# Kernel tuning notes

Measured on AMD Instinct MI355X. Metric: run time of the kernel, lower is better.

The kernel has to match this reference:

```python
import jax, jax.numpy as jnp
import numpy as np

H, D = 16, 1024
HD = D // H  # 64

def setup_inputs() -> dict:
    key = jax.random.key(0)
    ks = jax.random.split(key, 11)
    B, S = 2, 2048
    s_in = 1.0 / np.sqrt(D)
    return {
        "V": jax.random.normal(ks[0], (B, S, D), jnp.float32),
        "K": jax.random.normal(ks[1], (B, S, D), jnp.float32),
        "Q": jax.random.normal(ks[2], (B, S, D), jnp.float32),
        # stacked per-head Linear weights, torch layout [out,in] -> [H, HD, D]
        "Wv": jax.random.normal(ks[3], (H, HD, D), jnp.float32) * s_in,
        "bv": jnp.zeros((H, HD), jnp.float32),
        "Wk": jax.random.normal(ks[4], (H, HD, D), jnp.float32) * s_in,
        "bk": jnp.zeros((H, HD), jnp.float32),
        "Wq": jax.random.normal(ks[5], (H, HD, D), jnp.float32) * s_in,
        "bq": jnp.zeros((H, HD), jnp.float32),
        "Wo": jax.random.normal(ks[6], (D, D), jnp.float32) * s_in,
        "bo": jnp.zeros((D,), jnp.float32),
    }

def reference(V, K, Q, Wv, bv, Wk, bk, Wq, bq, Wo, bo):
    scale = HD ** (-0.5)
    # per-head projections fused into one batched GEMM: [B,S,D] x [H,HD,D] -> [B,H,S,HD]
    q = jnp.einsum('bsd,hed->bhse', Q, Wq) + bq[None, :, None, :]
    k = jnp.einsum('bsd,hed->bhse', K, Wk) + bk[None, :, None, :]
    v = jnp.einsum('bsd,hed->bhse', V, Wv) + bv[None, :, None, :]
    # scaled dot-product attention
    scores = jnp.einsum('bhqe,bhke->bhqk', q, k) * scale  # [B,H,S,S]
    p = jax.nn.softmax(scores, axis=-1)
    att = jnp.einsum('bhqk,bhke->bhqe', p, v)  # [B,H,S,HD]
    # concat heads (head 0 first, matching the torch cat order) then output proj
    B, _, S, _ = att.shape
    cat = jnp.transpose(att, (0, 2, 1, 3)).reshape(B, S, H * HD)
    return cat @ Wo.T + bo
```

## Files before the change

### kernel.cpp

```cpp
#include <hip/hip_runtime.h>
#include <cstdint>
#include <cstddef>

typedef __bf16 bf16_t;
typedef bf16_t bf16x8 __attribute__((ext_vector_type(8)));
typedef float f32x4 __attribute__((ext_vector_type(4)));

__device__ __forceinline__ void gl_lds16(const void* g, void* l) {
  __builtin_amdgcn_global_load_lds(
      (const __attribute__((address_space(1))) void*)g,
      (__attribute__((address_space(3))) void*)l, 16, 0, 0);
}

__device__ __forceinline__ f32x4 mfma16(bf16x8 a, bf16x8 b, f32x4 c) {
  return __builtin_amdgcn_mfma_f32_16x16x32_bf16(a, b, c, 0, 0, 0);
}

struct CvtWArgs { const float* src[4]; };

__global__ __launch_bounds__(256) void convert_w(CvtWArgs a, bf16_t* __restrict__ dst) {
  unsigned g = blockIdx.x * 256u + threadIdx.x;
  unsigned seg = g >> 17, off = g & 0x1FFFFu;
  const float4* s = (const float4*)a.src[seg] + (size_t)off * 2;
  float4 x0 = s[0], x1 = s[1];
  bf16x8 o;
  o[0] = (bf16_t)x0.x; o[1] = (bf16_t)x0.y; o[2] = (bf16_t)x0.z; o[3] = (bf16_t)x0.w;
  o[4] = (bf16_t)x1.x; o[5] = (bf16_t)x1.y; o[6] = (bf16_t)x1.z; o[7] = (bf16_t)x1.w;
  *(bf16x8*)(dst + (size_t)g * 8) = o;
}

struct ProjArgs {
  const float* A[3]; const bf16_t* W[3]; const float* bias[3];
  bf16_t* out[3]; float scale[3];
};

__global__ __launch_bounds__(256, 3) void gemm_proj(ProjArgs p) {
  __shared__ __attribute__((aligned(16))) unsigned char smem[49152];
  float*  a_s = (float*)smem;
  bf16_t* b_s = (bf16_t*)(smem + 32768);
  const int K = 1024;
  const int z = blockIdx.z;
  const float*  A = p.A[z] + (size_t)blockIdx.x * 128 * K;
  const bf16_t* W = p.W[z] + (size_t)blockIdx.y * 128 * K;

  const int t = threadIdx.x;
  const int w = t >> 6, l = t & 63;
  const int lq = l >> 4, lr = l & 15;
  const int mq = w & 1, nq = w >> 1;

  f32x4 acc[4][4];
  f32x4 zero = {0.f, 0.f, 0.f, 0.f};
  #pragma unroll
  for (int i = 0; i < 4; i++)
    #pragma unroll
    for (int j = 0; j < 4; j++) acc[i][j] = zero;

  for (int k0 = 0; k0 < K; k0 += 64) {
    __syncthreads();
    #pragma unroll
    for (int i = 0; i < 8; i++) {
      int ci = t + i * 256;
      int r = ci >> 4, pc = ci & 15;
      int lc = pc ^ (r & 7);
      gl_lds16(A + (size_t)r * K + k0 + lc * 4, a_s + i * 1024 + w * 256);
    }
    #pragma unroll
    for (int i = 0; i < 4; i++) {
      int g = t + i * 256;
      int r = g >> 3, pc = g & 7;
      int lc = pc ^ (r & 7);
      gl_lds16(W + (size_t)r * K + k0 + lc * 8, b_s + i * 2048 + w * 512);
    }
    __syncthreads();
    #pragma unroll
    for (int kk = 0; kk < 2; kk++) {
      bf16x8 af[4], bfr[4];
      #pragma unroll
      for (int i = 0; i < 4; i++) {
        int R = mq * 64 + i * 16 + lr;
        int rx = R & 7;
        int c0 = kk * 8 + lq * 2;
        f32x4 lo = *(const f32x4*)(a_s + R * 64 + ((c0 ^ rx) << 2));
        f32x4 hi = *(const f32x4*)(a_s + R * 64 + (((c0 + 1) ^ rx) << 2));
        bf16x8 v;
        v[0] = (bf16_t)lo[0]; v[1] = (bf16_t)lo[1]; v[2] = (bf16_t)lo[2]; v[3] = (bf16_t)lo[3];
        v[4] = (bf16_t)hi[0]; v[5] = (bf16_t)hi[1]; v[6] = (bf16_t)hi[2]; v[7] = (bf16_t)hi[3];
        af[i] = v;
      }
      #pragma unroll
      for (int j = 0; j < 4; j++) {
        int R = nq * 64 + j * 16 + lr;
        int ch = (kk * 4 + lq) ^ (R & 7);
        bfr[j] = *(const bf16x8*)(b_s + R * 64 + ch * 8);
      }
      #pragma unroll
      for (int i = 0; i < 4; i++)
        #pragma unroll
        for (int j = 0; j < 4; j++)
          acc[i][j] = mfma16(af[i], bfr[j], acc[i][j]);
    }
  }

  const float* bias = p.bias[z];
  const float scale = p.scale[z];
  __syncthreads();
  bf16_t* ts = (bf16_t*)smem;
  #pragma unroll
  for (int i = 0; i < 4; i++) {
    #pragma unroll
    for (int j = 0; j < 4; j++) {
      int nl = nq * 64 + j * 16 + lr;
      float bz = bias[blockIdx.y * 128 + nl];
      #pragma unroll
      for (int r = 0; r < 4; r++) {
        int ml = mq * 64 + i * 16 + lq * 4 + r;
        bf16_t val = (bf16_t)((acc[i][j][r] + bz) * scale);
        if (z == 0) ts[nl * 136 + ml] = val;
        else        ts[ml * 136 + nl] = val;
      }
    }
  }
  __syncthreads();
  bf16_t* out = p.out[z];
  const int b = blockIdx.x >> 4, sbase = (blockIdx.x & 15) * 128;
  if (z == 0) {
    #pragma unroll
    for (int ii = 0; ii < 8; ii++) {
      int idx = t * 8 + ii * 2048;
      int rr = idx >> 7, cc = idx & 127;
      int n = blockIdx.y * 128 + rr;
      int h = n >> 6, e = n & 63;
      bf16x8 vq = *(const bf16x8*)(ts + rr * 136 + cc);
      *(bf16x8*)(out + ((size_t)(b * 16 + h) * 64 + e) * 2048 + sbase + cc) = vq;
    }
  } else {
    #pragma unroll
    for (int ii = 0; ii < 8; ii++) {
      int idx = t * 8 + ii * 2048;
      int rr = idx >> 7, cc = idx & 127;
      int n = blockIdx.y * 128 + cc;
      int h = n >> 6, e = n & 63;
      bf16x8 vq = *(const bf16x8*)(ts + rr * 136 + cc);
      *(bf16x8*)(out + ((size_t)(b * 16 + h) * 2048 + sbase + rr) * 64 + e) = vq;
    }
  }
}

__global__ __launch_bounds__(256, 2) void attn(
    const bf16_t* __restrict__ qw, const bf16_t* __restrict__ kw,
    const bf16_t* __restrict__ vtw, bf16_t* __restrict__ att)
{
  __shared__ bf16_t qp_s[128 * 64];
  __shared__ bf16_t k_s[64 * 64];
  __shared__ bf16_t v_s[64 * 64];
  const int bh = blockIdx.y, qt = blockIdx.x;
  const int t = threadIdx.x, w = t >> 6, l = t & 63, lq = l >> 4, lr = l & 15;
  const int lr7 = lr & 7, lrh = lr >> 3;

  const bf16_t* qbase = qw + ((size_t)bh * 2048 + qt * 128) * 64;
  #pragma unroll
  for (int i = 0; i < 4; i++) {
    int oe = t * 8 + i * 2048;
    int r = oe >> 6;
    int lc = ((oe >> 3) & 7) ^ (r & 7);
    gl_lds16(qbase + r * 64 + lc * 8, qp_s + i * 2048 + w * 512);
  }
  __syncthreads();
  bf16x8 qf[2][2];
  #pragma unroll
  for (int i = 0; i < 2; i++)
    #pragma unroll
    for (int kk = 0; kk < 2; kk++) {
      int R = w * 32 + i * 16 + lr;
      int ch = (kk * 4 + lq) ^ lr7;
      qf[i][kk] = *(const bf16x8*)(qp_s + R * 64 + ch * 8);
    }

  f32x4 O[2][4];
  float lp[2][4];
  f32x4 zero = {0.f, 0.f, 0.f, 0.f};
  #pragma unroll
  for (int i = 0; i < 2; i++) {
    #pragma unroll
    for (int et = 0; et < 4; et++) O[i][et] = zero;
    #pragma unroll
    for (int r = 0; r < 4; r++) lp[i][r] = 0.f;
  }

  for (int kt = 0; kt < 32; ++kt) {
    __syncthreads();
    const bf16_t* kbase = kw + ((size_t)bh * 2048 + kt * 64) * 64;
    const bf16_t* vbase = vtw + (size_t)bh * 131072 + (size_t)kt * 64;
    #pragma unroll
    for (int i = 0; i < 2; i++) {
      int oe = t * 8 + i * 2048;
      int r = oe >> 6;
      int lc = ((oe >> 3) & 7) ^ (r & 7);
      gl_lds16(kbase + r * 64 + lc * 8, k_s + i * 2048 + w * 512);
      gl_lds16(vbase + (size_t)r * 2048 + lc * 8, v_s + i * 2048 + w * 512);
    }
    __syncthreads();

    f32x4 sc[2][4];
    #pragma unroll
    for (int i = 0; i < 2; i++)
      #pragma unroll
      for (int j = 0; j < 4; j++) sc[i][j] = zero;
    #pragma unroll
    for (int kk = 0; kk < 2; kk++) {
      bf16x8 kf[4];
      #pragma unroll
      for (int j = 0; j < 4; j++) {
        int R = j * 16 + lr;
        int ch = (kk * 4 + lq) ^ lr7;
        kf[j] = *(const bf16x8*)(k_s + R * 64 + ch * 8);
      }
      #pragma unroll
      for (int i = 0; i < 2; i++)
        #pragma unroll
        for (int j = 0; j < 4; j++)
          sc[i][j] = mfma16(qf[i][kk], kf[j], sc[i][j]);
    }

    #pragma unroll
    for (int i = 0; i < 2; i++) {
      #pragma unroll
      for (int r = 0; r < 4; r++) {
        float p0 = __expf(sc[i][0][r]);
        float p1 = __expf(sc[i][1][r]);
        float p2 = __expf(sc[i][2][r]);
        float p3 = __expf(sc[i][3][r]);
        lp[i][r] += (p0 + p1) + (p2 + p3);
        int row = w * 32 + i * 16 + lq * 4 + r;
        int rx = row & 7;
        bf16_t* pr = qp_s + row * 64 + lr7;
        pr[(((0 + lrh) ^ rx) << 3)] = (bf16_t)p0;
        pr[(((2 + lrh) ^ rx) << 3)] = (bf16_t)p1;
        pr[(((4 + lrh) ^ rx) << 3)] = (bf16_t)p2;
        pr[(((6 + lrh) ^ rx) << 3)] = (bf16_t)p3;
      }
    }

    #pragma unroll
    for (int kk = 0; kk < 2; kk++) {
      bf16x8 pf[2], vf[4];
      #pragma unroll
      for (int i = 0; i < 2; i++) {
        int R = w * 32 + i * 16 + lr;
        int ch = (kk * 4 + lq) ^ lr7;
        pf[i] = *(const bf16x8*)(qp_s + R * 64 + ch * 8);
      }
      #pragma unroll
      for (int et = 0; et < 4; et++) {
        int R = et * 16 + lr;
        int ch = (kk * 4 + lq) ^ lr7;
        vf[et] = *(const bf16x8*)(v_s + R * 64 + ch * 8);
      }
      #pragma unroll
      for (int i = 0; i < 2; i++)
        #pragma unroll
        for (int et = 0; et < 4; et++)
          O[i][et] = mfma16(pf[i], vf[et], O[i][et]);
    }
  }

  const int b = bh >> 4, h = bh & 15;
  #pragma unroll
  for (int i = 0; i < 2; i++)
    #pragma unroll
    for (int r = 0; r < 4; r++) {
      float s = lp[i][r];
      s += __shfl_xor(s, 1);
      s += __shfl_xor(s, 2);
      s += __shfl_xor(s, 4);
      s += __shfl_xor(s, 8);
      float rinv = 1.0f / s;
      int row = qt * 128 + w * 32 + i * 16 + lq * 4 + r;
      #pragma unroll
      for (int et = 0; et < 4; et++) {
        int col = h * 64 + et * 16 + lr;
        att[((size_t)b * 2048 + row) * 1024 + col] = (bf16_t)(O[i][et][r] * rinv);
      }
    }
}

__global__ __launch_bounds__(256, 2) void gemm_out(
    const bf16_t* __restrict__ A, const bf16_t* __restrict__ W,
    const float* __restrict__ bias, float* __restrict__ out)
{
  __shared__ bf16_t a_s[64 * 64];
  __shared__ bf16_t b_s[128 * 64];
  const int K = 1024;
  const bf16_t* Ab = A + (size_t)blockIdx.y * 64 * K;
  const bf16_t* Wb = W + (size_t)blockIdx.x * 128 * K;
  const int t = threadIdx.x, w = t >> 6, l = t & 63, lq = l >> 4, lr = l & 15;
  const int mh = w & 1, nh = w >> 1;

  f32x4 acc[2][4];
  f32x4 zero = {0.f, 0.f, 0.f, 0.f};
  #pragma unroll
  for (int i = 0; i < 2; i++)
    #pragma unroll
    for (int j = 0; j < 4; j++) acc[i][j] = zero;

  for (int k0 = 0; k0 < K; k0 += 64) {
    __syncthreads();
    #pragma unroll
    for (int i = 0; i < 2; i++) {
      int g = t + i * 256;
      int r = g >> 3, pc = g & 7;
      int lc = pc ^ (r & 7);
      gl_lds16(Ab + (size_t)r * K + k0 + lc * 8, a_s + i * 2048 + w * 512);
    }
    #pragma unroll
    for (int i = 0; i < 4; i++) {
      int g = t + i * 256;
      int r = g >> 3, pc = g & 7;
      int lc = pc ^ (r & 7);
      gl_lds16(Wb + (size_t)r * K + k0 + lc * 8, b_s + i * 2048 + w * 512);
    }
    __syncthreads();
    #pragma unroll
    for (int kk = 0; kk < 2; kk++) {
      bf16x8 af[2], bfr[4];
      #pragma unroll
      for (int i = 0; i < 2; i++) {
        int R = mh * 32 + i * 16 + lr;
        int ch = (kk * 4 + lq) ^ (R & 7);
        af[i] = *(const bf16x8*)(a_s + R * 64 + ch * 8);
      }
      #pragma unroll
      for (int j = 0; j < 4; j++) {
        int R = nh * 64 + j * 16 + lr;
        int ch = (kk * 4 + lq) ^ (R & 7);
        bfr[j] = *(const bf16x8*)(b_s + R * 64 + ch * 8);
      }
      #pragma unroll
      for (int i = 0; i < 2; i++)
        #pragma unroll
        for (int j = 0; j < 4; j++)
          acc[i][j] = mfma16(af[i], bfr[j], acc[i][j]);
    }
  }

  #pragma unroll
  for (int i = 0; i < 2; i++) {
    #pragma unroll
    for (int j = 0; j < 4; j++) {
      int col = blockIdx.x * 128 + nh * 64 + j * 16 + lr;
      float bz = bias[col];
      #pragma unroll
      for (int r = 0; r < 4; r++) {
        int row = blockIdx.y * 64 + mh * 32 + i * 16 + lq * 4 + r;
        out[(size_t)row * 1024 + col] = acc[i][j][r] + bz;
      }
    }
  }
}

extern "C" void kernel_launch(void* const* d_in, const int* in_sizes, int n_in,
                              void* d_out, int out_size, void* d_ws, size_t ws_size,
                              hipStream_t stream) {
  (void)in_sizes; (void)n_in; (void)out_size;
  const float* V  = (const float*)d_in[0];
  const float* Kx = (const float*)d_in[1];
  const float* Q  = (const float*)d_in[2];
  const float* Wv = (const float*)d_in[3];
  const float* bv = (const float*)d_in[4];
  const float* Wk = (const float*)d_in[5];
  const float* bk = (const float*)d_in[6];
  const float* Wq = (const float*)d_in[7];
  const float* bq = (const float*)d_in[8];
  const float* Wo = (const float*)d_in[9];
  const float* bo = (const float*)d_in[10];

  const size_t E = 1048576;
  if (ws_size < 20 * E * sizeof(bf16_t)) return;

  bf16_t* ws = (bf16_t*)d_ws;
  bf16_t* cWo   = ws;
  bf16_t* cWv   = ws + E;
  bf16_t* cWk   = ws + 2 * E;
  bf16_t* cWq   = ws + 3 * E;
  bf16_t* q_ws  = ws + 4 * E;
  bf16_t* k_ws  = ws + 8 * E;
  bf16_t* vt_ws = ws + 12 * E;
  bf16_t* att_ws= ws + 16 * E;

  CvtWArgs cw;
  cw.src[0] = Wo; cw.src[1] = Wv; cw.src[2] = Wk; cw.src[3] = Wq;
  convert_w<<<2048, 256, 0, stream>>>(cw, ws);

  ProjArgs pa;
  pa.A[0] = V;   pa.A[1] = Kx;  pa.A[2] = Q;
  pa.W[0] = cWv; pa.W[1] = cWk; pa.W[2] = cWq;
  pa.bias[0] = bv; pa.bias[1] = bk; pa.bias[2] = bq;
  pa.out[0] = vt_ws; pa.out[1] = k_ws; pa.out[2] = q_ws;
  pa.scale[0] = 1.f; pa.scale[1] = 1.f; pa.scale[2] = 0.125f;
  gemm_proj<<<dim3(32, 8, 3), 256, 0, stream>>>(pa);

  attn<<<dim3(16, 32), 256, 0, stream>>>(q_ws, k_ws, vt_ws, att_ws);

  gemm_out<<<dim3(8, 64), 256, 0, stream>>>(att_ws, cWo, bo, (float*)d_out);
}
```

Baseline: 234.1 us.

## Keep attention P in registers via transposed S^T and shrink query tile

Computes the score tile transposed (K·Q^T) so the exponentiated probabilities already sit in the MFMA B-operand layout and feed the PV MFMA directly from registers, removing the LDS write/read round-trip for P. The query tile per block drops from 128 to 64 rows, so the grid doubles and occupancy hints rise to 4 blocks per CU, with less LDS per block. The output is staged through a padded LDS tile so global stores become 16-byte coalesced rows. The trade-off is that K/V tiles are reloaded by twice as many blocks, and the V fragments are now assembled from two 8-byte LDS reads.

```diff
diff --git a/kernel.cpp b/kernel.cpp
--- a/kernel.cpp
+++ b/kernel.cpp
@@ -4,6 +4,7 @@
 
 typedef __bf16 bf16_t;
 typedef bf16_t bf16x8 __attribute__((ext_vector_type(8)));
+typedef bf16_t bf16x4 __attribute__((ext_vector_type(4)));
 typedef float f32x4 __attribute__((ext_vector_type(4)));
 
 __device__ __forceinline__ void gl_lds16(const void* g, void* l) {
@@ -146,46 +147,38 @@
   }
 }
 
-__global__ __launch_bounds__(256, 2) void attn(
+__global__ __launch_bounds__(256, 4) void attn(
     const bf16_t* __restrict__ qw, const bf16_t* __restrict__ kw,
     const bf16_t* __restrict__ vtw, bf16_t* __restrict__ att)
 {
-  __shared__ bf16_t qp_s[128 * 64];
   __shared__ bf16_t k_s[64 * 64];
   __shared__ bf16_t v_s[64 * 64];
+  __shared__ bf16_t qe_s[64 * 72];
   const int bh = blockIdx.y, qt = blockIdx.x;
   const int t = threadIdx.x, w = t >> 6, l = t & 63, lq = l >> 4, lr = l & 15;
-  const int lr7 = lr & 7, lrh = lr >> 3;
-
-  const bf16_t* qbase = qw + ((size_t)bh * 2048 + qt * 128) * 64;
-  #pragma unroll
-  for (int i = 0; i < 4; i++) {
-    int oe = t * 8 + i * 2048;
-    int r = oe >> 6;
-    int lc = ((oe >> 3) & 7) ^ (r & 7);
-    gl_lds16(qbase + r * 64 + lc * 8, qp_s + i * 2048 + w * 512);
+
+  const bf16_t* qbase = qw + ((size_t)bh * 2048 + qt * 64) * 64;
+  #pragma unroll
+  for (int i = 0; i < 2; i++) {
+    int g = t + i * 256;
+    int r = g >> 3, pc = g & 7;
+    int lc = pc ^ (r & 7);
+    gl_lds16(qbase + (size_t)r * 64 + lc * 8, qe_s + i * 2048 + w * 512);
   }
   __syncthreads();
-  bf16x8 qf[2][2];
-  #pragma unroll
-  for (int i = 0; i < 2; i++)
-    #pragma unroll
-    for (int kk = 0; kk < 2; kk++) {
-      int R = w * 32 + i * 16 + lr;
-      int ch = (kk * 4 + lq) ^ lr7;
-      qf[i][kk] = *(const bf16x8*)(qp_s + R * 64 + ch * 8);
-    }
-
-  f32x4 O[2][4];
-  float lp[2][4];
+  bf16x8 qf[2];
+  #pragma unroll
+  for (int kk = 0; kk < 2; kk++) {
+    int R = w * 16 + lr;
+    int ch = (kk * 4 + lq) ^ (R & 7);
+    qf[kk] = *(const bf16x8*)(qe_s + R * 64 + ch * 8);
+  }
+
+  f32x4 O[4];
   f32x4 zero = {0.f, 0.f, 0.f, 0.f};
   #pragma unroll
-  for (int i = 0; i < 2; i++) {
-    #pragma unroll
-    for (int et = 0; et < 4; et++) O[i][et] = zero;
-    #pragma unroll
-    for (int r = 0; r < 4; r++) lp[i][r] = 0.f;
-  }
+  for (int et = 0; et < 4; et++) O[et] = zero;
+  float lsum = 0.f;
 
   for (int kt = 0; kt < 32; ++kt) {
     __syncthreads();
@@ -193,95 +186,81 @@
     const bf16_t* vbase = vtw + (size_t)bh * 131072 + (size_t)kt * 64;
     #pragma unroll
     for (int i = 0; i < 2; i++) {
-      int oe = t * 8 + i * 2048;
-      int r = oe >> 6;
-      int lc = ((oe >> 3) & 7) ^ (r & 7);
-      gl_lds16(kbase + r * 64 + lc * 8, k_s + i * 2048 + w * 512);
+      int g = t + i * 256;
+      int r = g >> 3, pc = g & 7;
+      int lc = pc ^ (r & 7);
+      gl_lds16(kbase + (size_t)r * 64 + lc * 8, k_s + i * 2048 + w * 512);
       gl_lds16(vbase + (size_t)r * 2048 + lc * 8, v_s + i * 2048 + w * 512);
     }
     __syncthreads();
 
-    f32x4 sc[2][4];
-    #pragma unroll
-    for (int i = 0; i < 2; i++)
-      #pragma unroll
-      for (int j = 0; j < 4; j++) sc[i][j] = zero;
+    f32x4 sc[4];
+    #pragma unroll
+    for (int j = 0; j < 4; j++) sc[j] = zero;
     #pragma unroll
     for (int kk = 0; kk < 2; kk++) {
-      bf16x8 kf[4];
       #pragma unroll
       for (int j = 0; j < 4; j++) {
         int R = j * 16 + lr;
-        int ch = (kk * 4 + lq) ^ lr7;
-        kf[j] = *(const bf16x8*)(k_s + R * 64 + ch * 8);
-      }
-      #pragma unroll
-      for (int i = 0; i < 2; i++)
-        #pragma unroll
-        for (int j = 0; j < 4; j++)
-          sc[i][j] = mfma16(qf[i][kk], kf[j], sc[i][j]);
-    }
-
-    #pragma unroll
-    for (int i = 0; i < 2; i++) {
+        int ch = (kk * 4 + lq) ^ (R & 7);
+        bf16x8 kf = *(const bf16x8*)(k_s + R * 64 + ch * 8);
+        sc[j] = mfma16(kf, qf[kk], sc[j]);
+      }
+    }
+
+    bf16x8 pb[2];
+    #pragma unroll
+    for (int ks2 = 0; ks2 < 2; ks2++) {
       #pragma unroll
       for (int r = 0; r < 4; r++) {
-        float p0 = __expf(sc[i][0][r]);
-        float p1 = __expf(sc[i][1][r]);
-        float p2 = __expf(sc[i][2][r]);
-        float p3 = __expf(sc[i][3][r]);
-        lp[i][r] += (p0 + p1) + (p2 + p3);
-        int row = w * 32 + i * 16 + lq * 4 + r;
-        int rx = row & 7;
-        bf16_t* pr = qp_s + row * 64 + lr7;
-        pr[(((0 + lrh) ^ rx) << 3)] = (bf16_t)p0;
-        pr[(((2 + lrh) ^ rx) << 3)] = (bf16_t)p1;
-        pr[(((4 + lrh) ^ rx) << 3)] = (bf16_t)p2;
-        pr[(((6 + lrh) ^ rx) << 3)] = (bf16_t)p3;
-      }
-    }
-
-    #pragma unroll
-    for (int kk = 0; kk < 2; kk++) {
-      bf16x8 pf[2], vf[4];
-      #pragma unroll
-      for (int i = 0; i < 2; i++) {
-        int R = w * 32 + i * 16 + lr;
-        int ch = (kk * 4 + lq) ^ lr7;
-        pf[i] = *(const bf16x8*)(qp_s + R * 64 + ch * 8);
-      }
+        float e0 = __expf(sc[2 * ks2][r]);
+        float e1 = __expf(sc[2 * ks2 + 1][r]);
+        lsum += e0 + e1;
+        pb[ks2][r] = (bf16_t)e0;
+        pb[ks2][4 + r] = (bf16_t)e1;
+      }
+    }
+
+    #pragma unroll
+    for (int ks2 = 0; ks2 < 2; ks2++) {
       #pragma unroll
       for (int et = 0; et < 4; et++) {
         int R = et * 16 + lr;
-        int ch = (kk * 4 + lq) ^ lr7;
-        vf[et] = *(const bf16x8*)(v_s + R * 64 + ch * 8);
-      }
-      #pragma unroll
-      for (int i = 0; i < 2; i++)
-        #pragma unroll
-        for (int et = 0; et < 4; et++)
-          O[i][et] = mfma16(pf[i], vf[et], O[i][et]);
-    }
-  }
-
+        int rx = R & 7;
+        int ch0 = (ks2 * 4 + (lq >> 1)) ^ rx;
+        int ch1 = (ks2 * 4 + 2 + (lq >> 1)) ^ rx;
+        int half = (lq & 1) * 4;
+        bf16x4 vlo = *(const bf16x4*)(v_s + R * 64 + ch0 * 8 + half);
+        bf16x4 vhi = *(const bf16x4*)(v_s + R * 64 + ch1 * 8 + half);
+        bf16x8 vf;
+        vf[0] = vlo[0]; vf[1] = vlo[1]; vf[2] = vlo[2]; vf[3] = vlo[3];
+        vf[4] = vhi[0]; vf[5] = vhi[1]; vf[6] = vhi[2]; vf[7] = vhi[3];
+        O[et] = mfma16(vf, pb[ks2], O[et]);
+      }
+    }
+  }
+
+  float s = lsum;
+  s += __shfl_xor(s, 16);
+  s += __shfl_xor(s, 32);
+  float rinv = 1.0f / s;
+
+  #pragma unroll
+  for (int et = 0; et < 4; et++) {
+    bf16x4 pv;
+    #pragma unroll
+    for (int r = 0; r < 4; r++) pv[r] = (bf16_t)(O[et][r] * rinv);
+    *(bf16x4*)(qe_s + (w * 16 + lr) * 72 + et * 16 + lq * 4) = pv;
+  }
+  __syncthreads();
   const int b = bh >> 4, h = bh & 15;
   #pragma unroll
-  for (int i = 0; i < 2; i++)
-    #pragma unroll
-    for (int r = 0; r < 4; r++) {
-      float s = lp[i][r];
-      s += __shfl_xor(s, 1);
-      s += __shfl_xor(s, 2);
-      s += __shfl_xor(s, 4);
-      s += __shfl_xor(s, 8);
-      float rinv = 1.0f / s;
-      int row = qt * 128 + w * 32 + i * 16 + lq * 4 + r;
-      #pragma unroll
-      for (int et = 0; et < 4; et++) {
-        int col = h * 64 + et * 16 + lr;
-        att[((size_t)b * 2048 + row) * 1024 + col] = (bf16_t)(O[i][et][r] * rinv);
-      }
-    }
+  for (int i = 0; i < 2; i++) {
+    int c = t + i * 256;
+    int row = c >> 3, c8 = c & 7;
+    bf16x8 vv = *(const bf16x8*)(qe_s + row * 72 + c8 * 8);
+    *(bf16x8*)(att + ((size_t)b * 2048 + qt * 64 + row) * 1024 + h * 64 + c8 * 8) = vv;
+  }
 }
 
 __global__ __launch_bounds__(256, 2) void gemm_out(
@@ -399,7 +378,7 @@
   pa.scale[0] = 1.f; pa.scale[1] = 1.f; pa.scale[2] = 0.125f;
   gemm_proj<<<dim3(32, 8, 3), 256, 0, stream>>>(pa);
 
-  attn<<<dim3(16, 32), 256, 0, stream>>>(q_ws, k_ws, vt_ws, att_ws);
+  attn<<<dim3(32, 32), 256, 0, stream>>>(q_ws, k_ws, vt_ws, att_ws);
 
   gemm_out<<<dim3(8, 64), 256, 0, stream>>>(att_ws, cWo, bo, (float*)d_out);
 }
```

Measured after the change: 225.3 us. 1.04x faster.
